# Kernel tuning notes

Hardware: AMD Instinct MI355X
Metric: run time of the kernel (lower is better)

## Reference

```python
import jax, jax.numpy as jnp
import numpy as np
import math

HIDDEN = 2048
HEADS = 16
HEAD_DIM = HIDDEN // HEADS
MAX_SEQ = 2048
BATCH = 2
SEQ = 2048


def _rope_tables(seq_len, dim):
    inv_freq = 1.0 / (10000.0 ** (np.arange(0, dim, 2, dtype=np.float32) / dim))
    t = np.arange(seq_len, dtype=np.float32)
    freqs = np.einsum('i,j->ij', t, inv_freq)  # [S, dim/2]
    emb = np.concatenate([freqs, freqs], axis=-1)  # [S, dim]
    return jnp.asarray(np.cos(emb)), jnp.asarray(np.sin(emb))


def setup_inputs() -> dict:
    key = jax.random.key(0)
    ks = jax.random.split(key, 5)
    s = 1.0 / math.sqrt(HIDDEN)
    x = jax.random.normal(ks[0], (BATCH, SEQ, HIDDEN), dtype=jnp.float32)
    Wq = jax.random.normal(ks[1], (HIDDEN, HIDDEN), dtype=jnp.float32) * s
    Wk = jax.random.normal(ks[2], (HIDDEN, HIDDEN), dtype=jnp.float32) * s
    Wv = jax.random.normal(ks[3], (HIDDEN, HIDDEN), dtype=jnp.float32) * s
    Wo = jax.random.normal(ks[4], (HIDDEN, HIDDEN), dtype=jnp.float32) * s
    return {"x": x, "Wq": Wq, "Wk": Wk, "Wv": Wv, "Wo": Wo}


def _rotate_half(t):
    t1, t2 = t[..., : t.shape[-1] // 2], t[..., t.shape[-1] // 2 :]
    return jnp.concatenate([-t2, t1], axis=-1)


def reference(x, Wq, Wk, Wv, Wo):
    b, s, _ = x.shape
    # nn.Linear: y = x @ W.T
    def proj(W):
        return jnp.einsum('bsd,hd->bsh', x, W).reshape(b, s, HEADS, HEAD_DIM).transpose(0, 2, 1, 3)
    q, k, v = proj(Wq), proj(Wk), proj(Wv)  # [b, H, s, hd]
    cos, sin = _rope_tables(s, HEAD_DIM)    # [s, hd]
    cos = cos[None, None]
    sin = sin[None, None]
    q = q * cos + _rotate_half(q) * sin
    k = k * cos + _rotate_half(k) * sin
    scale = 1.0 / math.sqrt(HEAD_DIM)
    scores = jnp.einsum('bhqd,bhkd->bhqk', q, k) * scale
    causal = jnp.triu(jnp.ones((s, s), dtype=bool), k=1)
    scores = jnp.where(causal[None, None], -jnp.inf, scores)
    attn = jax.nn.softmax(scores, axis=-1)
    out = jnp.einsum('bhqk,bhkd->bhqd', attn, v)
    out = out.transpose(0, 2, 1, 3).reshape(b, s, HIDDEN)
    return jnp.einsum('bsd,hd->bsh', out, Wo)
```

## Files before the change

### kernel.cpp

```cpp
#include <hip/hip_runtime.h>
#include <stdint.h>


#define SCALE_Q 0.08838834764831845f

typedef short bf16x8 __attribute__((ext_vector_type(8)));
typedef float f32x4 __attribute__((ext_vector_type(4)));
typedef unsigned short u16x4v __attribute__((ext_vector_type(4)));
typedef unsigned short u16x8v __attribute__((ext_vector_type(8)));

__device__ __forceinline__ unsigned short f2bf(float f) {
  unsigned u = __float_as_uint(f);
  return (unsigned short)((u + 0x7FFFu + ((u >> 16) & 1u)) >> 16);
}
__device__ __forceinline__ float bf2f(unsigned short h) {
  return __uint_as_float(((unsigned)h) << 16);
}
__device__ __forceinline__ void gld16(void* lds, const void* g) {
  __builtin_amdgcn_global_load_lds(
      (const __attribute__((address_space(1))) unsigned int*)g,
      (__attribute__((address_space(3))) unsigned int*)lds, 16, 0, 0);
}

__global__ __launch_bounds__(256) void cvt_all(
    const float* __restrict__ x, const float* __restrict__ wq,
    const float* __restrict__ wk, const float* __restrict__ wv,
    const float* __restrict__ wo,
    unsigned short* __restrict__ xb, unsigned short* __restrict__ wqkv,
    unsigned short* __restrict__ wob) {
  int r = blockIdx.y;
  size_t i = ((size_t)blockIdx.x * 256 + threadIdx.x) * 8;
  const float* src; unsigned short* dst; size_t n;
  if (r == 0)      { src = x;  dst = xb;             n = 8388608; }
  else if (r == 1) { src = wq; dst = wqkv;           n = 4194304; }
  else if (r == 2) { src = wk; dst = wqkv + 4194304; n = 4194304; }
  else if (r == 3) { src = wv; dst = wqkv + 8388608; n = 4194304; }
  else             { src = wo; dst = wob;            n = 4194304; }
  if (i >= n) return;
  float4 a = *(const float4*)(src + i);
  float4 b = *(const float4*)(src + i + 4);
  u16x8v o;
  o[0] = f2bf(a.x); o[1] = f2bf(a.y); o[2] = f2bf(a.z); o[3] = f2bf(a.w);
  o[4] = f2bf(b.x); o[5] = f2bf(b.y); o[6] = f2bf(b.z); o[7] = f2bf(b.w);
  *(u16x8v*)(dst + i) = o;
}

__global__ __launch_bounds__(256) void rope_table(float* __restrict__ ct, float* __restrict__ st) {
  int id = blockIdx.x * 256 + threadIdx.x;
  int s = id >> 6, j = id & 63;
  float inv = __powf(10000.0f, -(float)j * (1.0f / 64.0f));
  float a = (float)s * inv;
  ct[id] = __cosf(a);
  st[id] = __sinf(a);
}

__global__ __launch_bounds__(512, 2) void gemm8p2(
    const unsigned short* __restrict__ A, const unsigned short* __restrict__ B,
    void* __restrict__ C0, void* __restrict__ C1, void* __restrict__ C2,
    int N, int Kd, int nbx) {
  __shared__ unsigned short As[2][128 * 64];
  __shared__ unsigned short Bs[2][128 * 64];
  const int t = threadIdx.x;
  const int lane = t & 63, w = t >> 6;
  const int g = lane >> 4, c15 = lane & 15;
  const int wm = w >> 2, wn = w & 3;

  const int chunk = (int)blockIdx.x & 7;
  const int idx = (int)blockIdx.x >> 3;
  const int cpc = nbx >> 3;
  const int row = idx & 15;
  const int col = chunk * cpc + (idx >> 4);
  const int brow = row * 256, bcol = col * 256;

  const int l = t >> 3;
  const int lg = (t & 7) ^ (l & 7);
  const unsigned short* srcA = A + (size_t)(brow + l + ((lg >> 2) << 7)) * Kd + (lg & 3) * 8;
  const unsigned short* srcB = B + (size_t)(bcol + l + ((lg >> 2) << 7)) * Kd + (lg & 3) * 8;

  auto stage = [&](int kt) {
    const int buf = kt & 1;
    const unsigned short* a = srcA + kt * 32;
    const unsigned short* b = srcB + kt * 32;
    gld16((char*)As[buf] + t * 16, a);
    gld16((char*)As[buf] + 8192 + t * 16, a + (size_t)64 * Kd);
    gld16((char*)Bs[buf] + t * 16, b);
    gld16((char*)Bs[buf] + 8192 + t * 16, b + (size_t)64 * Kd);
  };

  const int aoff = c15 * 128 + ((((wm << 2) | g) ^ (c15 & 7)) << 4);
  const int boff = ((wn & 1) << 13) + c15 * 128 + (((((wn >> 1) << 2) | g) ^ (c15 & 7)) << 4);

  f32x4 zero4 = {0.f, 0.f, 0.f, 0.f};
  f32x4 acc[8][4];
#pragma unroll
  for (int a_ = 0; a_ < 8; ++a_)
#pragma unroll
    for (int b_ = 0; b_ < 4; ++b_) acc[a_][b_] = zero4;

  const int nk = Kd >> 5;
  stage(0);
  asm volatile("s_waitcnt vmcnt(0)" ::: "memory");
  __builtin_amdgcn_s_barrier();

  for (int kt = 0; kt < nk; ++kt) {
    const char* ab = (const char*)As[kt & 1];
    const char* bb = (const char*)Bs[kt & 1];
    bf16x8 bfv[4], af0[4], af1[4];
#pragma unroll
    for (int nj = 0; nj < 4; ++nj) bfv[nj] = *(const bf16x8*)(bb + boff + nj * 2048);
#pragma unroll
    for (int mi = 0; mi < 4; ++mi) af0[mi] = *(const bf16x8*)(ab + aoff + mi * 2048);
    __builtin_amdgcn_sched_barrier(0);
#pragma unroll
    for (int mi = 0; mi < 4; ++mi) af1[mi] = *(const bf16x8*)(ab + aoff + (mi + 4) * 2048);
    if (kt + 1 < nk) stage(kt + 1);
    asm volatile("s_waitcnt lgkmcnt(4)" ::: "memory");
    __builtin_amdgcn_sched_barrier(0);
    __builtin_amdgcn_s_setprio(1);
#pragma unroll
    for (int mi = 0; mi < 4; ++mi)
#pragma unroll
      for (int nj = 0; nj < 4; ++nj)
        acc[mi][nj] = __builtin_amdgcn_mfma_f32_16x16x32_bf16(
            af0[mi], bfv[nj], acc[mi][nj], 0, 0, 0);
    __builtin_amdgcn_s_setprio(0);
    asm volatile("s_waitcnt lgkmcnt(0)" ::: "memory");
    __builtin_amdgcn_sched_barrier(0);
    __builtin_amdgcn_s_setprio(1);
#pragma unroll
    for (int mi = 0; mi < 4; ++mi)
#pragma unroll
      for (int nj = 0; nj < 4; ++nj)
        acc[mi + 4][nj] = __builtin_amdgcn_mfma_f32_16x16x32_bf16(
            af1[mi], bfv[nj], acc[mi + 4][nj], 0, 0, 0);
    __builtin_amdgcn_s_setprio(0);
    asm volatile("s_waitcnt vmcnt(0)" ::: "memory");
    __builtin_amdgcn_s_barrier();
  }

#pragma unroll
  for (int mi = 0; mi < 8; ++mi) {
#pragma unroll
    for (int nj = 0; nj < 4; ++nj) {
      f32x4 v = acc[mi][nj];
      int row0 = brow + wm * 128 + mi * 16 + g * 4;
      int colc = bcol + wn * 64 + nj * 16 + c15;
      int which = colc >> 11;
      int hc = colc & 2047;
      int bh = ((row0 >> 11) << 4) + (hc >> 7);
      int d = hc & 127, s0 = row0 & 2047;
      if (which == 2) {
        u16x4v pk;
        pk[0] = f2bf(v[0]); pk[1] = f2bf(v[1]); pk[2] = f2bf(v[2]); pk[3] = f2bf(v[3]);
        *(u16x4v*)((unsigned short*)C2 + ((size_t)bh * 128 + d) * 2048 + s0) = pk;
      } else {
        unsigned short* dst =
            (unsigned short*)(which ? C1 : C0) + ((size_t)bh * 2048 + s0) * 128 + d;
#pragma unroll
        for (int i2 = 0; i2 < 4; ++i2) dst[(size_t)i2 * 128] = f2bf(v[i2]);
      }
    }
  }
}

__global__ __launch_bounds__(256) void gemm_bt(
    const unsigned short* __restrict__ A, const unsigned short* __restrict__ B,
    float* __restrict__ C, int N, int Kd) {
  __shared__ unsigned short As[128 * 64];
  __shared__ unsigned short Bs[128 * 64];
  const int t = threadIdx.x;
  const int lane = t & 63, w = t >> 6;
  const int g = lane >> 4, c15 = lane & 15;
  const int wr = w >> 1, wc = w & 1;
  const int brow = blockIdx.y * 128, bcol = blockIdx.x * 128;
  const int srow = t >> 3;
  const int ssl = (t & 7) ^ (srow & 7);
  const unsigned short* pA = A + (size_t)(brow + srow) * Kd + ssl * 8;
  const unsigned short* pB = B + (size_t)(bcol + srow) * Kd + ssl * 8;

  int aoff[4][2], boff[4][2];
#pragma unroll
  for (int mi = 0; mi < 4; ++mi)
#pragma unroll
    for (int kk = 0; kk < 2; ++kk) {
      int arow = wr * 64 + mi * 16 + c15;
      int bcolr = wc * 64 + mi * 16 + c15;
      int p = (kk * 4 + g) ^ (c15 & 7);
      aoff[mi][kk] = arow * 128 + (p << 4);
      boff[mi][kk] = bcolr * 128 + (p << 4);
    }
  f32x4 zero4 = {0.f, 0.f, 0.f, 0.f};
  f32x4 acc[4][4];
#pragma unroll
  for (int a_ = 0; a_ < 4; ++a_)
#pragma unroll
    for (int b_ = 0; b_ < 4; ++b_) acc[a_][b_] = zero4;

  const int nk = Kd >> 6;
  for (int kt = 0; kt < nk; ++kt) {
    const unsigned short* a0 = pA + kt * 64;
    const unsigned short* b0 = pB + kt * 64;
#pragma unroll
    for (int c = 0; c < 4; ++c) {
      gld16((char*)As + c * 4096 + t * 16, a0 + (size_t)c * 32 * Kd);
      gld16((char*)Bs + c * 4096 + t * 16, b0 + (size_t)c * 32 * Kd);
    }
    __syncthreads();
    bf16x8 af[4][2], bfv[4][2];
#pragma unroll
    for (int mi = 0; mi < 4; ++mi)
#pragma unroll
      for (int kk = 0; kk < 2; ++kk) {
        af[mi][kk] = *(const bf16x8*)((const char*)As + aoff[mi][kk]);
        bfv[mi][kk] = *(const bf16x8*)((const char*)Bs + boff[mi][kk]);
      }
#pragma unroll
    for (int mi = 0; mi < 4; ++mi)
#pragma unroll
      for (int nj = 0; nj < 4; ++nj)
#pragma unroll
        for (int kk = 0; kk < 2; ++kk)
          acc[mi][nj] = __builtin_amdgcn_mfma_f32_16x16x32_bf16(
              af[mi][kk], bfv[nj][kk], acc[mi][nj], 0, 0, 0);
    __syncthreads();
  }
#pragma unroll
  for (int mi = 0; mi < 4; ++mi)
#pragma unroll
    for (int nj = 0; nj < 4; ++nj) {
      f32x4 v = acc[mi][nj];
      int row0 = brow + wr * 64 + mi * 16 + g * 4;
      int colc = bcol + wc * 64 + nj * 16 + c15;
#pragma unroll
      for (int i = 0; i < 4; ++i) C[(size_t)(row0 + i) * N + colc] = v[i];
    }
}

__global__ __launch_bounds__(256) void rope_apply(
    unsigned short* __restrict__ Q, unsigned short* __restrict__ K,
    const float* __restrict__ ct, const float* __restrict__ st) {
  int id = blockIdx.x * 256 + threadIdx.x;
  int o = id & 7;
  int s = (id >> 3) & 2047;
  int bh = id >> 14;
  size_t base = ((size_t)bh * 2048 + s) * 128 + o * 8;
  u16x8v qlo = *(u16x8v*)(Q + base), qhi = *(u16x8v*)(Q + base + 64);
  u16x8v klo = *(u16x8v*)(K + base), khi = *(u16x8v*)(K + base + 64);
  const float* cp = ct + s * 64 + o * 8;
  const float* sp = st + s * 64 + o * 8;
#pragma unroll
  for (int j = 0; j < 8; ++j) {
    float c = cp[j], sn = sp[j];
    float ql = bf2f(qlo[j]), qh = bf2f(qhi[j]);
    qlo[j] = f2bf((ql * c - qh * sn) * SCALE_Q);
    qhi[j] = f2bf((qh * c + ql * sn) * SCALE_Q);
    float kl = bf2f(klo[j]), kh = bf2f(khi[j]);
    klo[j] = f2bf(kl * c - kh * sn);
    khi[j] = f2bf(kh * c + kl * sn);
  }
  *(u16x8v*)(Q + base) = qlo; *(u16x8v*)(Q + base + 64) = qhi;
  *(u16x8v*)(K + base) = klo; *(u16x8v*)(K + base + 64) = khi;
}

__global__ __launch_bounds__(256) void attn_fwd(
    const unsigned short* __restrict__ Qg, const unsigned short* __restrict__ Kg,
    const unsigned short* __restrict__ Vtg, unsigned short* __restrict__ Og) {
  __shared__ unsigned short Ks[2][64 * 128];
  __shared__ unsigned short Vs[2][64 * 128];
  __shared__ unsigned short Pl[4][16 * 88];
  const int t = threadIdx.x;
  const int lane = t & 63, w = t >> 6;
  const int g = lane >> 4, c15 = lane & 15;
  const int pair = blockIdx.x;
  const int bh = blockIdx.y;
  const int b = bh >> 4, h = bh & 15;

  const int ksrow = t >> 4;
  const int kssl = (t & 15) ^ ksrow;
  const unsigned short* kp = Kg + ((size_t)bh * 2048 + ksrow) * 128 + kssl * 8;
  const int vsrow = t >> 3;
  const int vssl = (t & 7) ^ (vsrow & 7);
  const unsigned short* vp = Vtg + ((size_t)bh * 128 + vsrow) * 2048 + vssl * 8;

  auto stageTile = [&](int buf, int tkv) {
#pragma unroll
    for (int c = 0; c < 4; ++c) {
      gld16((char*)Ks[buf] + c * 4096 + t * 16, kp + (size_t)(tkv * 64 + c * 16) * 128);
      gld16((char*)Vs[buf] + c * 4096 + t * 16, vp + (size_t)c * 32 * 2048 + tkv * 64);
    }
  };

  f32x4 zero4 = {0.f, 0.f, 0.f, 0.f};
  f32x4 o[8];
  float mrow[4], lrow[4];
  bf16x8 qf[4];

  auto computeTile = [&](int buf, int qb, int tkv) {
    const int q0 = qb * 64;
    const int qrow = q0 + w * 16;
    f32x4 sv[4];
    __builtin_amdgcn_s_setprio(1);
#pragma unroll
    for (int cb = 0; cb < 4; ++cb) {
      f32x4 z = zero4;
#pragma unroll
      for (int kf = 0; kf < 4; ++kf) {
        int rowk = cb * 16 + c15;
        int p = (kf * 4 + g) ^ c15;
        bf16x8 kfr = *(const bf16x8*)((const char*)Ks[buf] + rowk * 256 + p * 16);
        z = __builtin_amdgcn_mfma_f32_16x16x32_bf16(qf[kf], kfr, z, 0, 0, 0);
      }
      sv[cb] = z;
    }
    __builtin_amdgcn_s_setprio(0);
    if (tkv == qb) {
#pragma unroll
      for (int cb = 0; cb < 4; ++cb)
#pragma unroll
        for (int i = 0; i < 4; ++i) {
          int colk = q0 + cb * 16 + c15;
          int rq = qrow + g * 4 + i;
          if (colk > rq) sv[cb][i] = -1e30f;
        }
    }
    float pmx[4];
#pragma unroll
    for (int i = 0; i < 4; ++i)
      pmx[i] = fmaxf(fmaxf(sv[0][i], sv[1][i]), fmaxf(sv[2][i], sv[3][i]));
#pragma unroll
    for (int dd = 1; dd < 16; dd <<= 1)
#pragma unroll
      for (int i = 0; i < 4; ++i) pmx[i] = fmaxf(pmx[i], __shfl_xor(pmx[i], dd));
    float sc[4], psum[4];
#pragma unroll
    for (int i = 0; i < 4; ++i) {
      float nm = fmaxf(mrow[i], pmx[i]);
      sc[i] = __expf(mrow[i] - nm);
      mrow[i] = nm;
      psum[i] = 0.f;
    }
#pragma unroll
    for (int cb = 0; cb < 4; ++cb)
#pragma unroll
      for (int i = 0; i < 4; ++i) {
        float e = __expf(sv[cb][i] - mrow[i]);
        sv[cb][i] = e;
        psum[i] += e;
      }
#pragma unroll
    for (int dd = 1; dd < 16; dd <<= 1)
#pragma unroll
      for (int i = 0; i < 4; ++i) psum[i] += __shfl_xor(psum[i], dd);
#pragma unroll
    for (int i = 0; i < 4; ++i) lrow[i] = lrow[i] * sc[i] + psum[i];
#pragma unroll
    for (int db = 0; db < 8; ++db)
#pragma unroll
      for (int i = 0; i < 4; ++i) o[db][i] *= sc[i];

    unsigned short* pw = &Pl[w][0];
#pragma unroll
    for (int cb = 0; cb < 4; ++cb)
#pragma unroll
      for (int i = 0; i < 4; ++i)
        pw[(g * 4 + i) * 88 + cb * 16 + c15] = f2bf(sv[cb][i]);
    bf16x8 pf[2];
#pragma unroll
    for (int kb = 0; kb < 2; ++kb)
      pf[kb] = *(const bf16x8*)((const char*)pw + c15 * 176 + kb * 64 + g * 16);

    __builtin_amdgcn_s_setprio(1);
#pragma unroll
    for (int db = 0; db < 8; ++db) {
#pragma unroll
      for (int kb = 0; kb < 2; ++kb) {
        int rowv = db * 16 + c15;
        int p = (kb * 4 + g) ^ (c15 & 7);
        bf16x8 vfr = *(const bf16x8*)((const char*)Vs[buf] + rowv * 128 + p * 16);
        o[db] = __builtin_amdgcn_mfma_f32_16x16x32_bf16(pf[kb], vfr, o[db], 0, 0, 0);
      }
    }
    __builtin_amdgcn_s_setprio(0);
  };

  auto loadQ = [&](int qb) {
    const unsigned short* qp = Qg + ((size_t)bh * 2048 + qb * 64 + w * 16 + c15) * 128 + g * 8;
#pragma unroll
    for (int kf = 0; kf < 4; ++kf) qf[kf] = *(const bf16x8*)(qp + kf * 32);
#pragma unroll
    for (int db = 0; db < 8; ++db) o[db] = zero4;
#pragma unroll
    for (int i = 0; i < 4; ++i) { mrow[i] = -1e30f; lrow[i] = 0.f; }
  };

  auto writeO = [&](int qb) {
    float linv[4];
#pragma unroll
    for (int i = 0; i < 4; ++i) linv[i] = 1.0f / lrow[i];
#pragma unroll
    for (int db = 0; db < 8; ++db)
#pragma unroll
      for (int i = 0; i < 4; ++i) {
        int q = qb * 64 + w * 16 + g * 4 + i;
        Og[((size_t)(b * 2048 + q)) * 2048 + h * 128 + db * 16 + c15] =
            f2bf(o[db][i] * linv[i]);
      }
  };

  const int qbA = pair, qbB = 31 - pair;
  const int ntA = qbA + 1, ntB = qbB + 1;
  int cur = 0;

  stageTile(0, 0);
  loadQ(qbA);
  for (int tkv = 0; tkv < ntA; ++tkv) {
    __syncthreads();
    if (tkv + 1 < ntA) stageTile(cur ^ 1, tkv + 1);
    else               stageTile(cur ^ 1, 0);
    computeTile(cur, qbA, tkv);
    cur ^= 1;
  }
  writeO(qbA);
  loadQ(qbB);
  for (int tkv = 0; tkv < ntB; ++tkv) {
    __syncthreads();
    if (tkv + 1 < ntB) stageTile(cur ^ 1, tkv + 1);
    computeTile(cur, qbB, tkv);
    cur ^= 1;
  }
  writeO(qbB);
}

extern "C" void kernel_launch(void* const* d_in, const int* in_sizes, int n_in,
                              void* d_out, int out_size, void* d_ws, size_t ws_size,
                              hipStream_t stream) {
  const float* x  = (const float*)d_in[0];
  const float* Wq = (const float*)d_in[1];
  const float* Wk = (const float*)d_in[2];
  const float* Wv = (const float*)d_in[3];
  const float* Wo = (const float*)d_in[4];
  char* p = (char*)d_ws;
  unsigned short* xb    = (unsigned short*)p;
  unsigned short* wqkvb = (unsigned short*)(p + 16777216);
  unsigned short* wob   = (unsigned short*)(p + 41943040);
  unsigned short* Qb    = (unsigned short*)(p + 50331648);
  unsigned short* Kb    = (unsigned short*)(p + 67108864);
  unsigned short* Vt    = (unsigned short*)(p + 83886080);
  float* ctab           = (float*)(p + 100663296);
  float* stab           = (float*)(p + 101187584);
  unsigned short* Ao = xb;

  cvt_all<<<dim3(4096, 5), 256, 0, stream>>>(x, Wq, Wk, Wv, Wo, xb, wqkvb, wob);
  rope_table<<<512, 256, 0, stream>>>(ctab, stab);
  gemm8p2<<<384, 512, 0, stream>>>(xb, wqkvb, Qb, Kb, Vt, 6144, 2048, 24);
  rope_apply<<<2048, 256, 0, stream>>>(Qb, Kb, ctab, stab);
  attn_fwd<<<dim3(16, 32), 256, 0, stream>>>(Qb, Kb, Vt, Ao);
  gemm_bt<<<dim3(16, 32), 256, 0, stream>>>(Ao, wob, (float*)d_out, 2048, 2048);
}
```

Measured before the change: 297.1 us.

## Split QKV projection into separate QK and V GEMMs with four-stage LDS pipeline

The fused 384-block QKV GEMM becomes two kernels. One uses 256x256 tiles to write Q and K. The other uses 128x256 tiles to write transposed V, also launched with 256 blocks. The aim is to remove the partial second wave of blocks across the CUs. Both kernels move from double buffering to a 4-deep global_load_lds ring with graded vmcnt waits, to hide more global-load latency. The larger LDS footprint (128 KB per block for the QK kernel) likely allows only one block per CU, so some occupancy is lost, and there is an extra kernel launch.

```diff
diff --git a/kernel.cpp b/kernel.cpp
--- a/kernel.cpp
+++ b/kernel.cpp
@@ -54,12 +54,11 @@
   st[id] = __sinf(a);
 }
 
-__global__ __launch_bounds__(512, 2) void gemm8p2(
+__global__ __launch_bounds__(512, 2) void gemm_qk(
     const unsigned short* __restrict__ A, const unsigned short* __restrict__ B,
-    void* __restrict__ C0, void* __restrict__ C1, void* __restrict__ C2,
-    int N, int Kd, int nbx) {
-  __shared__ unsigned short As[2][128 * 64];
-  __shared__ unsigned short Bs[2][128 * 64];
+    unsigned short* __restrict__ Qo, unsigned short* __restrict__ Ko, int Kd) {
+  __shared__ unsigned short As[4][128 * 64];
+  __shared__ unsigned short Bs[4][128 * 64];
   const int t = threadIdx.x;
   const int lane = t & 63, w = t >> 6;
   const int g = lane >> 4, c15 = lane & 15;
@@ -67,9 +66,8 @@
 
   const int chunk = (int)blockIdx.x & 7;
   const int idx = (int)blockIdx.x >> 3;
-  const int cpc = nbx >> 3;
   const int row = idx & 15;
-  const int col = chunk * cpc + (idx >> 4);
+  const int col = chunk * 2 + (idx >> 4);
   const int brow = row * 256, bcol = col * 256;
 
   const int l = t >> 3;
@@ -78,7 +76,7 @@
   const unsigned short* srcB = B + (size_t)(bcol + l + ((lg >> 2) << 7)) * Kd + (lg & 3) * 8;
 
   auto stage = [&](int kt) {
-    const int buf = kt & 1;
+    const int buf = kt & 3;
     const unsigned short* a = srcA + kt * 32;
     const unsigned short* b = srcB + kt * 32;
     gld16((char*)As[buf] + t * 16, a);
@@ -98,13 +96,13 @@
     for (int b_ = 0; b_ < 4; ++b_) acc[a_][b_] = zero4;
 
   const int nk = Kd >> 5;
-  stage(0);
-  asm volatile("s_waitcnt vmcnt(0)" ::: "memory");
+  stage(0); stage(1); stage(2);
+  asm volatile("s_waitcnt vmcnt(8)" ::: "memory");
   __builtin_amdgcn_s_barrier();
 
   for (int kt = 0; kt < nk; ++kt) {
-    const char* ab = (const char*)As[kt & 1];
-    const char* bb = (const char*)Bs[kt & 1];
+    const char* ab = (const char*)As[kt & 3];
+    const char* bb = (const char*)Bs[kt & 3];
     bf16x8 bfv[4], af0[4], af1[4];
 #pragma unroll
     for (int nj = 0; nj < 4; ++nj) bfv[nj] = *(const bf16x8*)(bb + boff + nj * 2048);
@@ -113,7 +111,7 @@
     __builtin_amdgcn_sched_barrier(0);
 #pragma unroll
     for (int mi = 0; mi < 4; ++mi) af1[mi] = *(const bf16x8*)(ab + aoff + (mi + 4) * 2048);
-    if (kt + 1 < nk) stage(kt + 1);
+    if (kt + 3 < nk) stage(kt + 3);
     asm volatile("s_waitcnt lgkmcnt(4)" ::: "memory");
     __builtin_amdgcn_sched_barrier(0);
     __builtin_amdgcn_s_setprio(1);
@@ -134,7 +132,13 @@
         acc[mi + 4][nj] = __builtin_amdgcn_mfma_f32_16x16x32_bf16(
             af1[mi], bfv[nj], acc[mi + 4][nj], 0, 0, 0);
     __builtin_amdgcn_s_setprio(0);
-    asm volatile("s_waitcnt vmcnt(0)" ::: "memory");
+    if (kt + 3 < nk) {
+      asm volatile("s_waitcnt vmcnt(8)" ::: "memory");
+    } else if (kt + 2 < nk) {
+      asm volatile("s_waitcnt vmcnt(4)" ::: "memory");
+    } else if (kt + 1 < nk) {
+      asm volatile("s_waitcnt vmcnt(0)" ::: "memory");
+    }
     __builtin_amdgcn_s_barrier();
   }
 
@@ -149,16 +153,113 @@
       int hc = colc & 2047;
       int bh = ((row0 >> 11) << 4) + (hc >> 7);
       int d = hc & 127, s0 = row0 & 2047;
-      if (which == 2) {
-        u16x4v pk;
-        pk[0] = f2bf(v[0]); pk[1] = f2bf(v[1]); pk[2] = f2bf(v[2]); pk[3] = f2bf(v[3]);
-        *(u16x4v*)((unsigned short*)C2 + ((size_t)bh * 128 + d) * 2048 + s0) = pk;
-      } else {
-        unsigned short* dst =
-            (unsigned short*)(which ? C1 : C0) + ((size_t)bh * 2048 + s0) * 128 + d;
-#pragma unroll
-        for (int i2 = 0; i2 < 4; ++i2) dst[(size_t)i2 * 128] = f2bf(v[i2]);
-      }
+      unsigned short* dst =
+          (which ? Ko : Qo) + ((size_t)bh * 2048 + s0) * 128 + d;
+#pragma unroll
+      for (int i2 = 0; i2 < 4; ++i2) dst[(size_t)i2 * 128] = f2bf(v[i2]);
+    }
+  }
+}
+
+__global__ __launch_bounds__(512, 2) void gemm_v(
+    const unsigned short* __restrict__ A, const unsigned short* __restrict__ B,
+    unsigned short* __restrict__ Vt, int Kd) {
+  __shared__ unsigned short As[4][64 * 64];
+  __shared__ unsigned short Bs[4][128 * 64];
+  const int t = threadIdx.x;
+  const int lane = t & 63, w = t >> 6;
+  const int g = lane >> 4, c15 = lane & 15;
+  const int wm = w >> 2, wn = w & 3;
+
+  const int chunk = (int)blockIdx.x & 7;
+  const int idx = (int)blockIdx.x >> 3;
+  const int row = chunk * 4 + (idx >> 3);
+  const int col = idx & 7;
+  const int brow = row * 128, bcol = col * 256;
+
+  const int l = t >> 3;
+  const int lg = (t & 7) ^ (l & 7);
+  const unsigned short* srcA = A + (size_t)(brow + l + ((lg >> 2) << 6)) * Kd + (lg & 3) * 8;
+  const unsigned short* srcB = B + (size_t)(bcol + l + ((lg >> 2) << 7)) * Kd + (lg & 3) * 8;
+
+  auto stage = [&](int kt) {
+    const int buf = kt & 3;
+    const unsigned short* a = srcA + kt * 32;
+    const unsigned short* b = srcB + kt * 32;
+    gld16((char*)As[buf] + t * 16, a);
+    gld16((char*)Bs[buf] + t * 16, b);
+    gld16((char*)Bs[buf] + 8192 + t * 16, b + (size_t)64 * Kd);
+  };
+
+  const int aoff = c15 * 128 + ((((wm << 2) | g) ^ (c15 & 7)) << 4);
+  const int boff = ((wn & 1) << 13) + c15 * 128 + (((((wn >> 1) << 2) | g) ^ (c15 & 7)) << 4);
+
+  f32x4 zero4 = {0.f, 0.f, 0.f, 0.f};
+  f32x4 acc[4][4];
+#pragma unroll
+  for (int a_ = 0; a_ < 4; ++a_)
+#pragma unroll
+    for (int b_ = 0; b_ < 4; ++b_) acc[a_][b_] = zero4;
+
+  const int nk = Kd >> 5;
+  stage(0); stage(1); stage(2);
+  asm volatile("s_waitcnt vmcnt(6)" ::: "memory");
+  __builtin_amdgcn_s_barrier();
+
+  for (int kt = 0; kt < nk; ++kt) {
+    const char* ab = (const char*)As[kt & 3];
+    const char* bb = (const char*)Bs[kt & 3];
+    bf16x8 bfv[4], af0[2], af1[2];
+#pragma unroll
+    for (int nj = 0; nj < 4; ++nj) bfv[nj] = *(const bf16x8*)(bb + boff + nj * 2048);
+#pragma unroll
+    for (int mi = 0; mi < 2; ++mi) af0[mi] = *(const bf16x8*)(ab + aoff + mi * 2048);
+    __builtin_amdgcn_sched_barrier(0);
+#pragma unroll
+    for (int mi = 0; mi < 2; ++mi) af1[mi] = *(const bf16x8*)(ab + aoff + (mi + 2) * 2048);
+    if (kt + 3 < nk) stage(kt + 3);
+    asm volatile("s_waitcnt lgkmcnt(2)" ::: "memory");
+    __builtin_amdgcn_sched_barrier(0);
+    __builtin_amdgcn_s_setprio(1);
+#pragma unroll
+    for (int mi = 0; mi < 2; ++mi)
+#pragma unroll
+      for (int nj = 0; nj < 4; ++nj)
+        acc[mi][nj] = __builtin_amdgcn_mfma_f32_16x16x32_bf16(
+            af0[mi], bfv[nj], acc[mi][nj], 0, 0, 0);
+    __builtin_amdgcn_s_setprio(0);
+    asm volatile("s_waitcnt lgkmcnt(0)" ::: "memory");
+    __builtin_amdgcn_sched_barrier(0);
+    __builtin_amdgcn_s_setprio(1);
+#pragma unroll
+    for (int mi = 0; mi < 2; ++mi)
+#pragma unroll
+      for (int nj = 0; nj < 4; ++nj)
+        acc[mi + 2][nj] = __builtin_amdgcn_mfma_f32_16x16x32_bf16(
+            af1[mi], bfv[nj], acc[mi + 2][nj], 0, 0, 0);
+    __builtin_amdgcn_s_setprio(0);
+    if (kt + 3 < nk) {
+      asm volatile("s_waitcnt vmcnt(6)" ::: "memory");
+    } else if (kt + 3 == nk) {
+      asm volatile("s_waitcnt vmcnt(3)" ::: "memory");
+    } else if (kt + 2 == nk) {
+      asm volatile("s_waitcnt vmcnt(0)" ::: "memory");
+    }
+    __builtin_amdgcn_s_barrier();
+  }
+
+#pragma unroll
+  for (int mi = 0; mi < 4; ++mi) {
+#pragma unroll
+    for (int nj = 0; nj < 4; ++nj) {
+      f32x4 v = acc[mi][nj];
+      int row0 = brow + wm * 64 + mi * 16 + g * 4;
+      int colc = bcol + wn * 64 + nj * 16 + c15;
+      int bh = ((row0 >> 11) << 4) + (colc >> 7);
+      int d = colc & 127, s0 = row0 & 2047;
+      u16x4v pk;
+      pk[0] = f2bf(v[0]); pk[1] = f2bf(v[1]); pk[2] = f2bf(v[2]); pk[3] = f2bf(v[3]);
+      *(u16x4v*)(Vt + ((size_t)bh * 128 + d) * 2048 + s0) = pk;
     }
   }
 }
@@ -452,7 +553,8 @@
 
   cvt_all<<<dim3(4096, 5), 256, 0, stream>>>(x, Wq, Wk, Wv, Wo, xb, wqkvb, wob);
   rope_table<<<512, 256, 0, stream>>>(ctab, stab);
-  gemm8p2<<<384, 512, 0, stream>>>(xb, wqkvb, Qb, Kb, Vt, 6144, 2048, 24);
+  gemm_qk<<<256, 512, 0, stream>>>(xb, wqkvb, Qb, Kb, 2048);
+  gemm_v<<<256, 512, 0, stream>>>(xb, wqkvb + (size_t)4096 * 2048, Vt, 2048);
   rope_apply<<<2048, 256, 0, stream>>>(Qb, Kb, ctab, stab);
   attn_fwd<<<dim3(16, 32), 256, 0, stream>>>(Qb, Kb, Vt, Ao);
   gemm_bt<<<dim3(16, 32), 256, 0, stream>>>(Ao, wob, (float*)d_out, 2048, 2048);
```

Result: faster. 283.5 us (-4.6%).
